# Kernel optimization log

Measured on AMD Instinct MI355X. Metric: run time of the kernel, lower is better.

Reference implementation:

```python
import jax, jax.numpy as jnp
import numpy as np

N = 30000        # nodes
E = 300000       # edges (before self-loops)
B = 300          # graphs
EMB = 64         # emb_dim (inner_dim overwritten to emb_dim in __init__)
HEADS = 4
OUT3 = 121       # hard-coded in conv3
H3 = 6           # heads of conv3
NCLS = 10
NVOC = 5000      # node token vocab for node_encoder
MAXD = 64        # max node depth for node_encoder


def _p(k, shape, scale=0.1):
    return scale * jax.random.normal(k, shape, dtype=jnp.float32)


def setup_inputs() -> dict:
    key = jax.random.key(0)
    ks = jax.random.split(key, 20)
    inp = {}
    inp["x"] = jax.random.randint(ks[0], (N, 1), 0, NVOC, dtype=jnp.int32)
    inp["node_depth"] = jax.random.randint(ks[1], (N, 1), 0, MAXD, dtype=jnp.int32)
    inp["edge_index"] = jax.random.randint(ks[2], (2, E), 0, N, dtype=jnp.int32)
    inp["batch"] = jnp.sort(jax.random.randint(ks[3], (N,), 0, B, dtype=jnp.int32))
    # node_encoder params (token emb + depth emb)
    inp["node_emb"] = _p(ks[4], (NVOC, EMB))
    inp["depth_emb"] = _p(ks[5], (MAXD, EMB))
    d1 = HEADS * EMB
    inp["w1"] = _p(ks[6], (EMB, d1))
    inp["as1"] = _p(ks[7], (HEADS, EMB))
    inp["ad1"] = _p(ks[8], (HEADS, EMB))
    inp["b1"] = jnp.zeros((d1,), jnp.float32)
    inp["w2"] = _p(ks[9], (d1, d1))
    inp["as2"] = _p(ks[10], (HEADS, EMB))
    inp["ad2"] = _p(ks[11], (HEADS, EMB))
    inp["b2"] = jnp.zeros((d1,), jnp.float32)
    d3 = H3 * OUT3
    inp["w3"] = _p(ks[12], (d1, d3))
    inp["as3"] = _p(ks[13], (H3, OUT3))
    inp["ad3"] = _p(ks[14], (H3, OUT3))
    inp["b3"] = jnp.zeros((d3,), jnp.float32)
    inp["wp"] = _p(ks[15], (OUT3, NCLS))
    inp["bp"] = jnp.zeros((NCLS,), jnp.float32)
    return inp


def gat_conv(x, W, a_src, a_dst, bias, src, dst, heads, out_dim):
    """PyG GATConv (concat=True, self-loops already in src/dst)."""
    n = x.shape[0]
    h = (x @ W).reshape(n, heads, out_dim)          # [N,H,D]
    es = (h * a_src).sum(-1)                        # [N,H] per-node src logits
    ed = (h * a_dst).sum(-1)                        # [N,H]
    e = jax.nn.leaky_relu(es[src] + ed[dst], 0.2)   # [E,H]
    # segment softmax over destination nodes (every node has a self-loop)
    m = jax.ops.segment_max(e, dst, num_segments=n)
    ex = jnp.exp(e - m[dst])
    s = jax.ops.segment_sum(ex, dst, num_segments=n)
    alpha = ex / (s[dst] + 1e-16)                   # [E,H]
    out = jax.ops.segment_sum(h[src] * alpha[:, :, None], dst, num_segments=n)
    return out.reshape(n, heads * out_dim) + bias


def reference(x, node_depth, edge_index, batch, node_emb, depth_emb,
              w1, as1, ad1, b1, w2, as2, ad2, b2, w3, as3, ad3, b3, wp, bp):
    n = x.shape[0]
    loops = jnp.arange(n, dtype=edge_index.dtype)
    src = jnp.concatenate([edge_index[0], loops])
    dst = jnp.concatenate([edge_index[1], loops])
    # node_encoder: token embedding + depth embedding
    h = node_emb[x[:, 0]] + depth_emb[node_depth.reshape(-1)]
    h = jax.nn.elu(gat_conv(h, w1, as1, ad1, b1, src, dst, HEADS, EMB))
    h = jax.nn.elu(gat_conv(h, w2, as2, ad2, b2, src, dst, HEADS, EMB))
    h = gat_conv(h, w3, as3, ad3, b3, src, dst, H3, OUT3)   # [N, 726]
    # global mean pool over graphs
    sums = jax.ops.segment_sum(h, batch, num_segments=B)
    cnt = jax.ops.segment_sum(jnp.ones((n,), h.dtype), batch, num_segments=B)
    g = sums / jnp.maximum(cnt, 1.0)[:, None]               # [B, 726]
    g = g.reshape(-1, H3, OUT3).mean(axis=1)                # [B, 121]
    return g @ wp + bp                                      # [B, NCLS]
```

## Files before the change

kernel.cpp:

```cpp
#include <hip/hip_runtime.h>
#include <hip/hip_bf16.h>
#include <math.h>

#define NN   30000
#define NE   300000
#define ETOT 330000
#define NB   300
#define EMB  64
#define D1   256
#define H1   4
#define H3   6
#define O3   121
#define D3   726
#define NQ   60
#define N3   72
#define NCLS 10

typedef __attribute__((ext_vector_type(8))) short short8;
typedef __attribute__((ext_vector_type(4))) float floatx4;

static inline int ceil_div(int a, int b) { return (a + b - 1) / b; }

__device__ inline void split_bf16(float f, unsigned short& hi, unsigned short& lo) {
    __hip_bfloat16 h = __float2bfloat16(f);
    float fh = __bfloat162float(h);
    __hip_bfloat16 l = __float2bfloat16(f - fh);
    hi = __builtin_bit_cast(unsigned short, h);
    lo = __builtin_bit_cast(unsigned short, l);
}

__device__ inline float bf2f(unsigned short u) {
    return __builtin_bit_cast(float, (unsigned int)u << 16);
}

__device__ inline unsigned short f2bf(float f) {
    return __builtin_bit_cast(unsigned short, __float2bfloat16(f));
}

__device__ inline float lrelu(float v) { return v > 0.f ? v : 0.2f * v; }


__global__ void setup1_kernel(const int* __restrict__ x, const int* __restrict__ dep,
                              const float* __restrict__ nemb, const float* __restrict__ demb,
                              const float* __restrict__ w1,
                              unsigned short* __restrict__ H0hi, unsigned short* __restrict__ H0lo,
                              unsigned short* __restrict__ W1hi, unsigned short* __restrict__ W1lo,
                              int* __restrict__ cnt, float* __restrict__ G,
                              int* __restrict__ gs, int* __restrict__ ge) {
    int i = blockIdx.x * blockDim.x + threadIdx.x;
    if (i < NN * EMB) {
        int n = i >> 6, d = i & 63;
        float v = nemb[x[n] * EMB + d] + demb[dep[n] * EMB + d];
        split_bf16(v, H0hi[i], H0lo[i]);
    }
    if (i < NN) cnt[i] = 0;
    if (i < NB) { gs[i] = 0; ge[i] = 0; }
    if (i < NB * NCLS) G[i] = 0.f;
    if (i < EMB * D1) {
        int k = i / D1, n = i % D1;
        unsigned short h, l;
        split_bf16(w1[i], h, l);
        W1hi[n * EMB + k] = h;
        W1lo[n * EMB + k] = l;
    }
}


__global__ void setup2_kernel(const int* __restrict__ ei, const int* __restrict__ batch,
                              const float* __restrict__ w2, const float* __restrict__ w3,
                              const float* __restrict__ as3, const float* __restrict__ ad3,
                              const float* __restrict__ wp,
                              int* __restrict__ cnt, int* __restrict__ gs, int* __restrict__ ge,
                              unsigned short* __restrict__ W2b,
                              unsigned short* __restrict__ W3b) {
    int i = blockIdx.x * blockDim.x + threadIdx.x;
    if (i < ETOT) {
        int dst = (i < NE) ? ei[NE + i] : (i - NE);
        atomicAdd(&cnt[dst], 1);
    }
    if (i < NN) {
        int b = batch[i];
        if (i == 0 || batch[i - 1] != b) gs[b] = i;
        if (i == NN - 1 || batch[i + 1] != b) ge[b] = i + 1;
    }
    if (i < D1 * D1) {
        int k = i / D1, n = i % D1;
        W2b[n * D1 + k] = f2bf(w2[i]);
    }
    if (i < N3 * D1) {
        int n = i / D1, k = i % D1;
        float acc = 0.f;
        if (n < NQ) {
            int h = n / NCLS, c = n % NCLS;
            const float* wrow = w3 + (size_t)k * D3 + h * O3;
            for (int j = 0; j < O3; j++) acc += wrow[j] * wp[j * NCLS + c];
        } else if (n < NQ + H3) {
            int h = n - NQ;
            const float* wrow = w3 + (size_t)k * D3 + h * O3;
            for (int j = 0; j < O3; j++) acc += wrow[j] * as3[h * O3 + j];
        } else {
            int h = n - NQ - H3;
            const float* wrow = w3 + (size_t)k * D3 + h * O3;
            for (int j = 0; j < O3; j++) acc += wrow[j] * ad3[h * O3 + j];
        }
        W3b[i] = f2bf(acc);
    }
}

__global__ __launch_bounds__(1024) void scan_kernel(const int* __restrict__ cnt,
                                                    int* __restrict__ rowoff,
                                                    int* __restrict__ fillp) {
    const int CHUNK = 30;
    __shared__ int wsum[16];
    int tid = threadIdx.x;
    int base = tid * CHUNK;
    int pref[CHUNK];
    int local = 0;
    #pragma unroll
    for (int i = 0; i < CHUNK; i++) {
        int idx = base + i;
        int c = (idx < NN) ? cnt[idx] : 0;
        pref[i] = local;
        local += c;
    }
    int lane = tid & 63, wave = tid >> 6;
    int incl = local;
    #pragma unroll
    for (int off2 = 1; off2 < 64; off2 <<= 1) {
        int t = __shfl_up(incl, off2);
        if (lane >= off2) incl += t;
    }
    if (lane == 63) wsum[wave] = incl;
    __syncthreads();
    if (wave == 0 && lane < 16) {
        int ws = wsum[lane];
        #pragma unroll
        for (int off2 = 1; off2 < 16; off2 <<= 1) {
            int t = __shfl_up(ws, off2);
            if (lane >= off2) ws += t;
        }
        wsum[lane] = ws;
    }
    __syncthreads();
    int waveoff = (wave > 0) ? wsum[wave - 1] : 0;
    int texcl = waveoff + incl - local;
    #pragma unroll
    for (int i = 0; i < CHUNK; i++) {
        int idx = base + i;
        if (idx < NN) {
            int e = texcl + pref[i];
            rowoff[idx] = e;
            fillp[idx]  = e;
        }
    }
    if (tid == 1023) rowoff[NN] = texcl + local;
}

__global__ void fill_kernel(const int* __restrict__ ei, int* __restrict__ fillp,
                            int* __restrict__ csr) {
    int e = blockIdx.x * blockDim.x + threadIdx.x;
    if (e >= ETOT) return;
    int src, dst;
    if (e < NE) { src = ei[e]; dst = ei[NE + e]; }
    else        { src = e - NE; dst = e - NE; }
    int slot = atomicAdd(&fillp[dst], 1);
    csr[slot] = src;
}


#define LDA 40

template <int MODE, bool SPLIT>
__global__ __launch_bounds__(256) void gemm_mfma_kernel(
    const unsigned short* __restrict__ Ahi, const unsigned short* __restrict__ Alo,
    const unsigned short* __restrict__ Bhi, const unsigned short* __restrict__ Blo,
    unsigned short* __restrict__ Cbf, unsigned short* __restrict__ Qb,
    float* __restrict__ es, float* __restrict__ ed,
    const float* __restrict__ as_, const float* __restrict__ ad_,
    int M, int K, int N) {
    __shared__ unsigned short sAh[128 * LDA], sBh[128 * LDA];
    __shared__ unsigned short sAl[SPLIT ? 128 * LDA : 1], sBl[SPLIT ? 128 * LDA : 1];
    int tid = threadIdx.x;
    int lane = tid & 63, wave = tid >> 6;
    int wr = (wave >> 1) * 64, wc = (wave & 1) * 64;
    int quad = lane >> 4, mr = lane & 15;
    int row0 = blockIdx.y * 128, col0 = blockIdx.x * 128;

    floatx4 zero = {0.f, 0.f, 0.f, 0.f};
    floatx4 acc[4][4];
    #pragma unroll
    for (int i = 0; i < 4; i++)
        #pragma unroll
        for (int j = 0; j < 4; j++) acc[i][j] = zero;

    for (int k0 = 0; k0 < K; k0 += 32) {
        #pragma unroll
        for (int ch = 0; ch < 2; ch++) {
            int linear = (ch * 256 + tid) * 8;
            int r = linear >> 5, c = linear & 31;
            uint4 vh, vl;
            int gr = row0 + r;
            if (gr < M) {
                vh = *(const uint4*)(Ahi + (size_t)gr * K + k0 + c);
                if (SPLIT) vl = *(const uint4*)(Alo + (size_t)gr * K + k0 + c);
            } else { vh = uint4{0, 0, 0, 0}; vl = uint4{0, 0, 0, 0}; }
            *(uint4*)&sAh[r * LDA + c] = vh;
            if (SPLIT) *(uint4*)&sAl[r * LDA + c] = vl;
            int gn = col0 + r;
            if (gn < N) {
                vh = *(const uint4*)(Bhi + (size_t)gn * K + k0 + c);
                if (SPLIT) vl = *(const uint4*)(Blo + (size_t)gn * K + k0 + c);
            } else { vh = uint4{0, 0, 0, 0}; vl = uint4{0, 0, 0, 0}; }
            *(uint4*)&sBh[r * LDA + c] = vh;
            if (SPLIT) *(uint4*)&sBl[r * LDA + c] = vl;
        }
        __syncthreads();

        short8 ah[4], al[4], bh[4], bl[4];
        #pragma unroll
        for (int i = 0; i < 4; i++) {
            int ar = wr + i * 16 + mr;
            ah[i] = *(const short8*)&sAh[ar * LDA + quad * 8];
            if (SPLIT) al[i] = *(const short8*)&sAl[ar * LDA + quad * 8];
            int br = wc + i * 16 + mr;
            bh[i] = *(const short8*)&sBh[br * LDA + quad * 8];
            if (SPLIT) bl[i] = *(const short8*)&sBl[br * LDA + quad * 8];
        }
        #pragma unroll
        for (int i = 0; i < 4; i++)
            #pragma unroll
            for (int j = 0; j < 4; j++) {
                acc[i][j] = __builtin_amdgcn_mfma_f32_16x16x32_bf16(ah[i], bh[j], acc[i][j], 0, 0, 0);
                if (SPLIT) {
                    acc[i][j] = __builtin_amdgcn_mfma_f32_16x16x32_bf16(ah[i], bl[j], acc[i][j], 0, 0, 0);
                    acc[i][j] = __builtin_amdgcn_mfma_f32_16x16x32_bf16(al[i], bh[j], acc[i][j], 0, 0, 0);
                }
            }
        __syncthreads();
    }

    #pragma unroll
    for (int i = 0; i < 4; i++) {
        #pragma unroll
        for (int j = 0; j < 4; j++) {
            int gc = col0 + wc + j * 16 + mr;
            if (gc >= N) continue;
            int gr0 = row0 + wr + i * 16 + quad * 4;
            #pragma unroll
            for (int r = 0; r < 4; r++) {
                int gr = gr0 + r;
                if (gr >= M) continue;
                float v = acc[i][j][r];
                if (MODE == 0) {
                    Cbf[(size_t)gr * D1 + gc] = f2bf(v);
                } else {
                    if (gc < NQ)            Qb[(size_t)gr * NQ + gc] = f2bf(v);
                    else if (gc < NQ + H3)  es[(size_t)gr * H3 + (gc - NQ)] = v;
                    else                    ed[(size_t)gr * H3 + (gc - NQ - H3)] = v;
                }
            }
        }
    }

    if (MODE == 0) {
        int hx = 2 * blockIdx.x + (wave & 1);
        float asr[4], adr[4];
        #pragma unroll
        for (int j = 0; j < 4; j++) {
            asr[j] = as_[hx * 64 + j * 16 + mr];
            adr[j] = ad_[hx * 64 + j * 16 + mr];
        }
        #pragma unroll
        for (int i = 0; i < 4; i++) {
            #pragma unroll
            for (int r = 0; r < 4; r++) {
                float ps = 0.f, pd = 0.f;
                #pragma unroll
                for (int j = 0; j < 4; j++) {
                    float v = acc[i][j][r];
                    ps += v * asr[j];
                    pd += v * adr[j];
                }
                #pragma unroll
                for (int m2 = 8; m2 >= 1; m2 >>= 1) {
                    ps += __shfl_xor(ps, m2);
                    pd += __shfl_xor(pd, m2);
                }
                int gr = row0 + wr + i * 16 + quad * 4 + r;
                if (mr == 0 && gr < M) {
                    es[gr * 4 + hx] = ps;
                    ed[gr * 4 + hx] = pd;
                }
            }
        }
    }
}


__global__ __launch_bounds__(256) void aggregate12_kernel(
    const unsigned short* __restrict__ P, const float* __restrict__ es,
    const float* __restrict__ ed, const int* __restrict__ rowoff,
    const int* __restrict__ csr, const float* __restrict__ bias,
    unsigned short* __restrict__ outHi) {
    int wave = threadIdx.x >> 6, lane = threadIdx.x & 63;
    int wid = blockIdx.x * 4 + wave;
    int head = lane >> 4;
    int f0 = lane * 4;
    float bv0 = bias[f0], bv1 = bias[f0 + 1], bv2 = bias[f0 + 2], bv3 = bias[f0 + 3];
    #pragma unroll 1
    for (int t = 0; t < 4; t++) {
        int dst = wid * 4 + t;
        int s0 = rowoff[dst], s1 = rowoff[dst + 1];
        float edv = ed[dst * 4 + head];
        float sum = 0.f;
        float acc0 = 0.f, acc1 = 0.f, acc2 = 0.f, acc3 = 0.f;
        int s = s0;
        for (; s + 8 <= s1; s += 8) {
            int si[8];
            #pragma unroll
            for (int u = 0; u < 8; u++) si[u] = csr[s + u];
            float vv[8];
            ushort4 pp[8];
            #pragma unroll
            for (int u = 0; u < 8; u++) {
                vv[u] = es[si[u] * 4 + head] + edv;
                pp[u] = *(const ushort4*)(P + (size_t)si[u] * D1 + f0);
            }
            #pragma unroll
            for (int u = 0; u < 8; u++) {
                float e = __expf(lrelu(vv[u]));
                sum += e;
                acc0 += e * bf2f(pp[u].x);
                acc1 += e * bf2f(pp[u].y);
                acc2 += e * bf2f(pp[u].z);
                acc3 += e * bf2f(pp[u].w);
            }
        }
        for (; s + 4 <= s1; s += 4) {
            int sa = csr[s], sb = csr[s + 1], sc = csr[s + 2], sd = csr[s + 3];
            float va = es[sa * 4 + head] + edv;
            float vb = es[sb * 4 + head] + edv;
            float vc = es[sc * 4 + head] + edv;
            float vd = es[sd * 4 + head] + edv;
            ushort4 pa = *(const ushort4*)(P + (size_t)sa * D1 + f0);
            ushort4 pb = *(const ushort4*)(P + (size_t)sb * D1 + f0);
            ushort4 pc = *(const ushort4*)(P + (size_t)sc * D1 + f0);
            ushort4 pd = *(const ushort4*)(P + (size_t)sd * D1 + f0);
            float ea = __expf(lrelu(va));
            float eb = __expf(lrelu(vb));
            float ec = __expf(lrelu(vc));
            float ee = __expf(lrelu(vd));
            sum += (ea + eb) + (ec + ee);
            acc0 += ea * bf2f(pa.x) + eb * bf2f(pb.x) + ec * bf2f(pc.x) + ee * bf2f(pd.x);
            acc1 += ea * bf2f(pa.y) + eb * bf2f(pb.y) + ec * bf2f(pc.y) + ee * bf2f(pd.y);
            acc2 += ea * bf2f(pa.z) + eb * bf2f(pb.z) + ec * bf2f(pc.z) + ee * bf2f(pd.z);
            acc3 += ea * bf2f(pa.w) + eb * bf2f(pb.w) + ec * bf2f(pc.w) + ee * bf2f(pd.w);
        }
        for (; s + 2 <= s1; s += 2) {
            int sa = csr[s], sb = csr[s + 1];
            float va = es[sa * 4 + head] + edv;
            float vb = es[sb * 4 + head] + edv;
            ushort4 pa = *(const ushort4*)(P + (size_t)sa * D1 + f0);
            ushort4 pb = *(const ushort4*)(P + (size_t)sb * D1 + f0);
            float ea = __expf(lrelu(va));
            float eb = __expf(lrelu(vb));
            sum += ea + eb;
            acc0 += ea * bf2f(pa.x) + eb * bf2f(pb.x);
            acc1 += ea * bf2f(pa.y) + eb * bf2f(pb.y);
            acc2 += ea * bf2f(pa.z) + eb * bf2f(pb.z);
            acc3 += ea * bf2f(pa.w) + eb * bf2f(pb.w);
        }
        for (; s < s1; s++) {
            int sa = csr[s];
            float va = es[sa * 4 + head] + edv;
            ushort4 pa = *(const ushort4*)(P + (size_t)sa * D1 + f0);
            float ea = __expf(lrelu(va));
            sum += ea;
            acc0 += ea * bf2f(pa.x);
            acc1 += ea * bf2f(pa.y);
            acc2 += ea * bf2f(pa.z);
            acc3 += ea * bf2f(pa.w);
        }
        float inv = 1.f / sum;
        float a0 = acc0 * inv + bv0;
        float a1 = acc1 * inv + bv1;
        float a2 = acc2 * inv + bv2;
        float a3 = acc3 * inv + bv3;
        a0 = a0 > 0.f ? a0 : expm1f(a0);
        a1 = a1 > 0.f ? a1 : expm1f(a1);
        a2 = a2 > 0.f ? a2 : expm1f(a2);
        a3 = a3 > 0.f ? a3 : expm1f(a3);
        ushort4 hi4;
        hi4.x = f2bf(a0); hi4.y = f2bf(a1); hi4.z = f2bf(a2); hi4.w = f2bf(a3);
        *(ushort4*)(outHi + (size_t)dst * D1 + f0) = hi4;
    }
}


__global__ __launch_bounds__(256) void aggregate3q_kernel(
    const unsigned short* __restrict__ Qb, const float* __restrict__ es,
    const float* __restrict__ ed, const int* __restrict__ rowoff,
    const int* __restrict__ csr, const int* __restrict__ batch,
    float* __restrict__ G) {
    int wave = threadIdx.x >> 6, lane = threadIdx.x & 63;
    int wid = blockIdx.x * 4 + wave;
    bool act = lane < NQ;
    int h = act ? (lane / NCLS) : 0;
    int q = act ? lane : 0;
    #pragma unroll 1
    for (int t = 0; t < 4; t++) {
        int dst = wid * 4 + t;
        int b = batch[dst];
        int s0 = rowoff[dst], s1 = rowoff[dst + 1];
        float edv = act ? ed[dst * H3 + h] : 0.f;
        float sum = 0.f, acc = 0.f;
        int s = s0;
        for (; s + 8 <= s1; s += 8) {
            int si[8];
            #pragma unroll
            for (int u = 0; u < 8; u++) si[u] = csr[s + u];
            float vv[8], qq[8];
            #pragma unroll
            for (int u = 0; u < 8; u++) {
                vv[u] = es[si[u] * H3 + h] + edv;
                qq[u] = bf2f(Qb[(size_t)si[u] * NQ + q]);
            }
            #pragma unroll
            for (int u = 0; u < 8; u++) {
                float e = __expf(lrelu(vv[u]));
                sum += e;
                acc += e * qq[u];
            }
        }
        for (; s + 2 <= s1; s += 2) {
            int sa = csr[s], sb = csr[s + 1];
            float va = es[sa * H3 + h] + edv;
            float vb = es[sb * H3 + h] + edv;
            float qa = bf2f(Qb[(size_t)sa * NQ + q]);
            float qb = bf2f(Qb[(size_t)sb * NQ + q]);
            float ea = __expf(lrelu(va));
            float eb = __expf(lrelu(vb));
            sum += ea + eb;
            acc += ea * qa + eb * qb;
        }
        for (; s < s1; s++) {
            int sa = csr[s];
            float va = es[sa * H3 + h] + edv;
            float qa = bf2f(Qb[(size_t)sa * NQ + q]);
            float ea = __expf(lrelu(va));
            sum += ea;
            acc += ea * qa;
        }
        acc *= 1.f / sum;
        float av = act ? acc : 0.f;
        float tot = av;
        #pragma unroll
        for (int h2 = 1; h2 < H3; h2++) tot += __shfl(av, lane + h2 * NCLS);
        if (lane < NCLS) atomicAdd(&G[b * NCLS + lane], tot);
    }
}


__global__ __launch_bounds__(64) void final_kernel(
    const float* __restrict__ G, const int* __restrict__ gs, const int* __restrict__ ge,
    const float* __restrict__ b3, const float* __restrict__ wp,
    const float* __restrict__ bp, float* __restrict__ out) {
    int b = blockIdx.x, tid = threadIdx.x;
    if (tid >= NCLS) return;
    int cntn = ge[b] - gs[b];
    float o = bp[tid];
    if (cntn > 0) {
        float bt = 0.f;
        for (int k = 0; k < O3; k++) {
            float bs = 0.f;
            #pragma unroll
            for (int h = 0; h < H3; h++) bs += b3[h * O3 + k];
            bt += bs * wp[k * NCLS + tid];
        }
        o += G[b * NCLS + tid] / (6.f * (float)cntn) + bt * (1.f / 6.f);
    }
    out[b * NCLS + tid] = o;
}


extern "C" void kernel_launch(void* const* d_in, const int* in_sizes, int n_in,
                              void* d_out, int out_size, void* d_ws, size_t ws_size,
                              hipStream_t stream) {
    const int* x     = (const int*)d_in[0];
    const int* dep   = (const int*)d_in[1];
    const int* ei    = (const int*)d_in[2];
    const int* batch = (const int*)d_in[3];
    const float* nemb = (const float*)d_in[4];
    const float* demb = (const float*)d_in[5];
    const float* w1  = (const float*)d_in[6];
    const float* as1 = (const float*)d_in[7];
    const float* ad1 = (const float*)d_in[8];
    const float* b1  = (const float*)d_in[9];
    const float* w2  = (const float*)d_in[10];
    const float* as2 = (const float*)d_in[11];
    const float* ad2 = (const float*)d_in[12];
    const float* b2  = (const float*)d_in[13];
    const float* w3  = (const float*)d_in[14];
    const float* as3 = (const float*)d_in[15];
    const float* ad3 = (const float*)d_in[16];
    const float* b3  = (const float*)d_in[17];
    const float* wp  = (const float*)d_in[18];
    const float* bp  = (const float*)d_in[19];
    float* out = (float*)d_out;

    char* ws = (char*)d_ws;
    size_t off = 0;
    auto alloc = [&](size_t bytes) -> void* {
        void* p = ws + off;
        off += (bytes + 255) & ~(size_t)255;
        return p;
    };
    unsigned short* Hb   = (unsigned short*)alloc((size_t)NN * D1 * 2);
    unsigned short* H0lo = (unsigned short*)alloc((size_t)NN * EMB * 2);
    unsigned short* W1hi = (unsigned short*)alloc((size_t)D1 * EMB * 2);
    unsigned short* W1lo = (unsigned short*)alloc((size_t)D1 * EMB * 2);
    unsigned short* W2b  = (unsigned short*)alloc((size_t)D1 * D1 * 2);
    unsigned short* W3b  = (unsigned short*)alloc((size_t)N3 * D1 * 2);
    unsigned short* Pb   = (unsigned short*)alloc((size_t)NN * D1 * 2);
    unsigned short* Qb   = (unsigned short*)alloc(((size_t)NN * NQ + 64) * 2);
    float* G    = (float*)alloc((size_t)NB * NCLS * 4);
    float* es   = (float*)alloc((size_t)NN * 6 * 4);
    float* ed   = (float*)alloc((size_t)NN * 6 * 4);
    int* cnt    = (int*)alloc((size_t)NN * 4);
    int* rowoff = (int*)alloc((size_t)(NN + 1) * 4);
    int* fillp  = (int*)alloc((size_t)NN * 4);
    int* csr    = (int*)alloc((size_t)ETOT * 4);
    int* gs     = (int*)alloc((size_t)NB * 4);
    int* ge     = (int*)alloc((size_t)NB * 4);

    setup1_kernel<<<ceil_div(NN * EMB, 256), 256, 0, stream>>>(
        x, dep, nemb, demb, w1, Hb, H0lo, W1hi, W1lo, cnt, G, gs, ge);
    setup2_kernel<<<ceil_div(ETOT, 256), 256, 0, stream>>>(
        ei, batch, w2, w3, as3, ad3, wp, cnt, gs, ge, W2b, W3b);
    scan_kernel<<<1, 1024, 0, stream>>>(cnt, rowoff, fillp);
    fill_kernel<<<ceil_div(ETOT, 256), 256, 0, stream>>>(ei, fillp, csr);

    gemm_mfma_kernel<0, true><<<dim3(2, ceil_div(NN, 128)), 256, 0, stream>>>(
        Hb, H0lo, W1hi, W1lo, Pb, nullptr, es, ed, as1, ad1, NN, EMB, D1);
    aggregate12_kernel<<<NN / 16, 256, 0, stream>>>(Pb, es, ed, rowoff, csr, b1, Hb);

    gemm_mfma_kernel<0, false><<<dim3(2, ceil_div(NN, 128)), 256, 0, stream>>>(
        Hb, nullptr, W2b, nullptr, Pb, nullptr, es, ed, as2, ad2, NN, D1, D1);
    aggregate12_kernel<<<NN / 16, 256, 0, stream>>>(Pb, es, ed, rowoff, csr, b2, Hb);

    gemm_mfma_kernel<1, false><<<dim3(1, ceil_div(NN, 128)), 256, 0, stream>>>(
        Hb, nullptr, W3b, nullptr, nullptr, Qb, es, ed, nullptr, nullptr, NN, D1, N3);
    aggregate3q_kernel<<<NN / 16, 256, 0, stream>>>(Qb, es, ed, rowoff, csr, batch, G);

    final_kernel<<<NB, 64, 0, stream>>>(G, gs, ge, b3, wp, bp, out);
}
```

Baseline: 324.7 us.

## Split edges across half-waves in aggregation and fold final kernel into fill/aggregate

The layer 1/2 aggregation now has each half-wave process alternate edges with 8-wide bf16 loads per lane, then combines the two halves with a cross-lane shuffle. This doubles the number of edges in flight per wave and widens each memory access. Separately, the final pooling kernel and the G buffer are removed. The output is pre-initialised with bias terms inside fill_kernel, and aggregate3q atomically adds pre-scaled contributions straight into the output. This saves a launch and an intermediate buffer, at the cost of extra shuffles and idle lanes in the odd-edge tail.

```diff
diff --git a/kernel.cpp b/kernel.cpp
--- a/kernel.cpp
+++ b/kernel.cpp
@@ -17,6 +17,7 @@
 #define NCLS 10
 
 typedef __attribute__((ext_vector_type(8))) short short8;
+typedef __attribute__((ext_vector_type(8))) unsigned short ushort8;
 typedef __attribute__((ext_vector_type(4))) float floatx4;
 
 static inline int ceil_div(int a, int b) { return (a + b - 1) / b; }
@@ -45,7 +46,7 @@
                               const float* __restrict__ w1,
                               unsigned short* __restrict__ H0hi, unsigned short* __restrict__ H0lo,
                               unsigned short* __restrict__ W1hi, unsigned short* __restrict__ W1lo,
-                              int* __restrict__ cnt, float* __restrict__ G,
+                              int* __restrict__ cnt,
                               int* __restrict__ gs, int* __restrict__ ge) {
     int i = blockIdx.x * blockDim.x + threadIdx.x;
     if (i < NN * EMB) {
@@ -55,7 +56,6 @@
     }
     if (i < NN) cnt[i] = 0;
     if (i < NB) { gs[i] = 0; ge[i] = 0; }
-    if (i < NB * NCLS) G[i] = 0.f;
     if (i < EMB * D1) {
         int k = i / D1, n = i % D1;
         unsigned short h, l;
@@ -157,14 +157,33 @@
 }
 
 __global__ void fill_kernel(const int* __restrict__ ei, int* __restrict__ fillp,
-                            int* __restrict__ csr) {
+                            int* __restrict__ csr,
+                            const int* __restrict__ gs, const int* __restrict__ ge,
+                            const float* __restrict__ b3, const float* __restrict__ wp,
+                            const float* __restrict__ bp, float* __restrict__ out) {
     int e = blockIdx.x * blockDim.x + threadIdx.x;
-    if (e >= ETOT) return;
-    int src, dst;
-    if (e < NE) { src = ei[e]; dst = ei[NE + e]; }
-    else        { src = e - NE; dst = e - NE; }
-    int slot = atomicAdd(&fillp[dst], 1);
-    csr[slot] = src;
+    if (e < ETOT) {
+        int src, dst;
+        if (e < NE) { src = ei[e]; dst = ei[NE + e]; }
+        else        { src = e - NE; dst = e - NE; }
+        int slot = atomicAdd(&fillp[dst], 1);
+        csr[slot] = src;
+    } else if (e < ETOT + NB * NCLS) {
+        int idx = e - ETOT;
+        int b = idx / NCLS, c = idx % NCLS;
+        float o = bp[c];
+        if (ge[b] - gs[b] > 0) {
+            float bt = 0.f;
+            for (int k = 0; k < O3; k++) {
+                float bs = 0.f;
+                #pragma unroll
+                for (int h = 0; h < H3; h++) bs += b3[h * O3 + k];
+                bt += bs * wp[k * NCLS + c];
+            }
+            o += bt * (1.f / 6.f);
+        }
+        out[b * NCLS + c] = o;
+    }
 }
 
 
@@ -304,95 +323,71 @@
     unsigned short* __restrict__ outHi) {
     int wave = threadIdx.x >> 6, lane = threadIdx.x & 63;
     int wid = blockIdx.x * 4 + wave;
-    int head = lane >> 4;
-    int f0 = lane * 4;
-    float bv0 = bias[f0], bv1 = bias[f0 + 1], bv2 = bias[f0 + 2], bv3 = bias[f0 + 3];
+    int lane32 = lane & 31;
+    int half = lane >> 5;
+    int head = lane32 >> 3;
+    int f0 = lane32 * 8;
+    float bv[8];
+    #pragma unroll
+    for (int e2 = 0; e2 < 8; e2++) bv[e2] = bias[f0 + e2];
     #pragma unroll 1
     for (int t = 0; t < 4; t++) {
         int dst = wid * 4 + t;
         int s0 = rowoff[dst], s1 = rowoff[dst + 1];
         float edv = ed[dst * 4 + head];
         float sum = 0.f;
-        float acc0 = 0.f, acc1 = 0.f, acc2 = 0.f, acc3 = 0.f;
+        float acc[8] = {};
         int s = s0;
         for (; s + 8 <= s1; s += 8) {
-            int si[8];
-            #pragma unroll
-            for (int u = 0; u < 8; u++) si[u] = csr[s + u];
-            float vv[8];
-            ushort4 pp[8];
-            #pragma unroll
-            for (int u = 0; u < 8; u++) {
+            int si[4];
+            float vv[4];
+            ushort8 pp[4];
+            #pragma unroll
+            for (int u = 0; u < 4; u++) {
+                si[u] = csr[s + 2 * u + half];
                 vv[u] = es[si[u] * 4 + head] + edv;
-                pp[u] = *(const ushort4*)(P + (size_t)si[u] * D1 + f0);
-            }
-            #pragma unroll
-            for (int u = 0; u < 8; u++) {
+                pp[u] = *(const ushort8*)(P + (size_t)si[u] * D1 + f0);
+            }
+            #pragma unroll
+            for (int u = 0; u < 4; u++) {
                 float e = __expf(lrelu(vv[u]));
                 sum += e;
-                acc0 += e * bf2f(pp[u].x);
-                acc1 += e * bf2f(pp[u].y);
-                acc2 += e * bf2f(pp[u].z);
-                acc3 += e * bf2f(pp[u].w);
-            }
-        }
-        for (; s + 4 <= s1; s += 4) {
-            int sa = csr[s], sb = csr[s + 1], sc = csr[s + 2], sd = csr[s + 3];
-            float va = es[sa * 4 + head] + edv;
-            float vb = es[sb * 4 + head] + edv;
-            float vc = es[sc * 4 + head] + edv;
-            float vd = es[sd * 4 + head] + edv;
-            ushort4 pa = *(const ushort4*)(P + (size_t)sa * D1 + f0);
-            ushort4 pb = *(const ushort4*)(P + (size_t)sb * D1 + f0);
-            ushort4 pc = *(const ushort4*)(P + (size_t)sc * D1 + f0);
-            ushort4 pd = *(const ushort4*)(P + (size_t)sd * D1 + f0);
-            float ea = __expf(lrelu(va));
-            float eb = __expf(lrelu(vb));
-            float ec = __expf(lrelu(vc));
-            float ee = __expf(lrelu(vd));
-            sum += (ea + eb) + (ec + ee);
-            acc0 += ea * bf2f(pa.x) + eb * bf2f(pb.x) + ec * bf2f(pc.x) + ee * bf2f(pd.x);
-            acc1 += ea * bf2f(pa.y) + eb * bf2f(pb.y) + ec * bf2f(pc.y) + ee * bf2f(pd.y);
-            acc2 += ea * bf2f(pa.z) + eb * bf2f(pb.z) + ec * bf2f(pc.z) + ee * bf2f(pd.z);
-            acc3 += ea * bf2f(pa.w) + eb * bf2f(pb.w) + ec * bf2f(pc.w) + ee * bf2f(pd.w);
+                #pragma unroll
+                for (int j = 0; j < 8; j++) acc[j] += e * bf2f(pp[u][j]);
+            }
         }
         for (; s + 2 <= s1; s += 2) {
-            int sa = csr[s], sb = csr[s + 1];
-            float va = es[sa * 4 + head] + edv;
-            float vb = es[sb * 4 + head] + edv;
-            ushort4 pa = *(const ushort4*)(P + (size_t)sa * D1 + f0);
-            ushort4 pb = *(const ushort4*)(P + (size_t)sb * D1 + f0);
-            float ea = __expf(lrelu(va));
-            float eb = __expf(lrelu(vb));
-            sum += ea + eb;
-            acc0 += ea * bf2f(pa.x) + eb * bf2f(pb.x);
-            acc1 += ea * bf2f(pa.y) + eb * bf2f(pb.y);
-            acc2 += ea * bf2f(pa.z) + eb * bf2f(pb.z);
-            acc3 += ea * bf2f(pa.w) + eb * bf2f(pb.w);
-        }
-        for (; s < s1; s++) {
+            int sa = csr[s + half];
+            float v = es[sa * 4 + head] + edv;
+            ushort8 p = *(const ushort8*)(P + (size_t)sa * D1 + f0);
+            float e = __expf(lrelu(v));
+            sum += e;
+            #pragma unroll
+            for (int j = 0; j < 8; j++) acc[j] += e * bf2f(p[j]);
+        }
+        if (s < s1) {
             int sa = csr[s];
-            float va = es[sa * 4 + head] + edv;
-            ushort4 pa = *(const ushort4*)(P + (size_t)sa * D1 + f0);
-            float ea = __expf(lrelu(va));
-            sum += ea;
-            acc0 += ea * bf2f(pa.x);
-            acc1 += ea * bf2f(pa.y);
-            acc2 += ea * bf2f(pa.z);
-            acc3 += ea * bf2f(pa.w);
-        }
-        float inv = 1.f / sum;
-        float a0 = acc0 * inv + bv0;
-        float a1 = acc1 * inv + bv1;
-        float a2 = acc2 * inv + bv2;
-        float a3 = acc3 * inv + bv3;
-        a0 = a0 > 0.f ? a0 : expm1f(a0);
-        a1 = a1 > 0.f ? a1 : expm1f(a1);
-        a2 = a2 > 0.f ? a2 : expm1f(a2);
-        a3 = a3 > 0.f ? a3 : expm1f(a3);
-        ushort4 hi4;
-        hi4.x = f2bf(a0); hi4.y = f2bf(a1); hi4.z = f2bf(a2); hi4.w = f2bf(a3);
-        *(ushort4*)(outHi + (size_t)dst * D1 + f0) = hi4;
+            float v = es[sa * 4 + head] + edv;
+            ushort8 p = *(const ushort8*)(P + (size_t)sa * D1 + f0);
+            float e = (half == 0) ? __expf(lrelu(v)) : 0.f;
+            sum += e;
+            #pragma unroll
+            for (int j = 0; j < 8; j++) acc[j] += e * bf2f(p[j]);
+        }
+        sum += __shfl_xor(sum, 32);
+        #pragma unroll
+        for (int j = 0; j < 8; j++) acc[j] += __shfl_xor(acc[j], 32);
+        if (half == 0) {
+            float inv = 1.f / sum;
+            ushort8 o;
+            #pragma unroll
+            for (int j = 0; j < 8; j++) {
+                float v = acc[j] * inv + bv[j];
+                v = v > 0.f ? v : expm1f(v);
+                o[j] = f2bf(v);
+            }
+            *(ushort8*)(outHi + (size_t)dst * D1 + f0) = o;
+        }
     }
 }
 
@@ -401,7 +396,8 @@
     const unsigned short* __restrict__ Qb, const float* __restrict__ es,
     const float* __restrict__ ed, const int* __restrict__ rowoff,
     const int* __restrict__ csr, const int* __restrict__ batch,
-    float* __restrict__ G) {
+    const int* __restrict__ gs, const int* __restrict__ ge,
+    float* __restrict__ out) {
     int wave = threadIdx.x >> 6, lane = threadIdx.x & 63;
     int wid = blockIdx.x * 4 + wave;
     bool act = lane < NQ;
@@ -456,30 +452,12 @@
         float tot = av;
         #pragma unroll
         for (int h2 = 1; h2 < H3; h2++) tot += __shfl(av, lane + h2 * NCLS);
-        if (lane < NCLS) atomicAdd(&G[b * NCLS + lane], tot);
-    }
-}
-
-
-__global__ __launch_bounds__(64) void final_kernel(
-    const float* __restrict__ G, const int* __restrict__ gs, const int* __restrict__ ge,
-    const float* __restrict__ b3, const float* __restrict__ wp,
-    const float* __restrict__ bp, float* __restrict__ out) {
-    int b = blockIdx.x, tid = threadIdx.x;
-    if (tid >= NCLS) return;
-    int cntn = ge[b] - gs[b];
-    float o = bp[tid];
-    if (cntn > 0) {
-        float bt = 0.f;
-        for (int k = 0; k < O3; k++) {
-            float bs = 0.f;
-            #pragma unroll
-            for (int h = 0; h < H3; h++) bs += b3[h * O3 + k];
-            bt += bs * wp[k * NCLS + tid];
-        }
-        o += G[b * NCLS + tid] / (6.f * (float)cntn) + bt * (1.f / 6.f);
-    }
-    out[b * NCLS + tid] = o;
+        if (lane < NCLS) {
+            int cntb = ge[b] - gs[b];
+            float scale = 1.f / (6.f * (float)(cntb > 0 ? cntb : 1));
+            atomicAdd(&out[b * NCLS + lane], tot * scale);
+        }
+    }
 }
 
 
@@ -523,7 +501,6 @@
     unsigned short* W3b  = (unsigned short*)alloc((size_t)N3 * D1 * 2);
     unsigned short* Pb   = (unsigned short*)alloc((size_t)NN * D1 * 2);
     unsigned short* Qb   = (unsigned short*)alloc(((size_t)NN * NQ + 64) * 2);
-    float* G    = (float*)alloc((size_t)NB * NCLS * 4);
     float* es   = (float*)alloc((size_t)NN * 6 * 4);
     float* ed   = (float*)alloc((size_t)NN * 6 * 4);
     int* cnt    = (int*)alloc((size_t)NN * 4);
@@ -534,11 +511,12 @@
     int* ge     = (int*)alloc((size_t)NB * 4);
 
     setup1_kernel<<<ceil_div(NN * EMB, 256), 256, 0, stream>>>(
-        x, dep, nemb, demb, w1, Hb, H0lo, W1hi, W1lo, cnt, G, gs, ge);
+        x, dep, nemb, demb, w1, Hb, H0lo, W1hi, W1lo, cnt, gs, ge);
     setup2_kernel<<<ceil_div(ETOT, 256), 256, 0, stream>>>(
         ei, batch, w2, w3, as3, ad3, wp, cnt, gs, ge, W2b, W3b);
     scan_kernel<<<1, 1024, 0, stream>>>(cnt, rowoff, fillp);
-    fill_kernel<<<ceil_div(ETOT, 256), 256, 0, stream>>>(ei, fillp, csr);
+    fill_kernel<<<ceil_div(ETOT + NB * NCLS, 256), 256, 0, stream>>>(
+        ei, fillp, csr, gs, ge, b3, wp, bp, out);
 
     gemm_mfma_kernel<0, true><<<dim3(2, ceil_div(NN, 128)), 256, 0, stream>>>(
         Hb, H0lo, W1hi, W1lo, Pb, nullptr, es, ed, as1, ad1, NN, EMB, D1);
@@ -550,7 +528,5 @@
 
     gemm_mfma_kernel<1, false><<<dim3(1, ceil_div(NN, 128)), 256, 0, stream>>>(
         Hb, nullptr, W3b, nullptr, nullptr, Qb, es, ed, nullptr, nullptr, NN, D1, N3);
-    aggregate3q_kernel<<<NN / 16, 256, 0, stream>>>(Qb, es, ed, rowoff, csr, batch, G);
-
-    final_kernel<<<NB, 64, 0, stream>>>(G, gs, ge, b3, wp, bp, out);
-}
+    aggregate3q_kernel<<<NN / 16, 256, 0, stream>>>(Qb, es, ed, rowoff, csr, batch, gs, ge, out);
+}
```

Result: no change. 328.6 us (+1.2%).
